# Kernel optimization log

Hardware: AMD Instinct MI355X
Metric: run time of the kernel (lower is better)

The kernel has to match this reference:

```python
import jax, jax.numpy as jnp
import numpy as np

NUM_HEADS = 16
NUM_KV_HEADS = 4
HEAD_DIM = 128
WINDOW = 1024  # sliding window: key j visible to query i iff 0 <= i - j <= WINDOW
SCALE = 0.08838834764831845  # 1/sqrt(HEAD_DIM)
NEG_INF = -1e30


def setup_inputs() -> dict:
    key = jax.random.key(0)
    k1, k2, k3, k4 = jax.random.split(key, 4)
    B, S = 4, 2048
    T = B * S
    return {
        "q": jax.random.normal(k1, (T, NUM_HEADS * HEAD_DIM), dtype=jnp.float32),
        "k": jax.random.normal(k2, (T, NUM_KV_HEADS * HEAD_DIM), dtype=jnp.float32),
        "v": jax.random.normal(k3, (T, NUM_KV_HEADS * HEAD_DIM), dtype=jnp.float32),
        "sinks": jax.random.normal(k4, (NUM_HEADS,), dtype=jnp.float32),
        "batch": B,
        "seqlen": S,
    }


def reference(q, k, v, sinks, batch, seqlen):
    """Varlen causal sliding-window attention with learnable per-head sink logits.

    Equal-length sequences: total_tokens = batch * seqlen, matching
    cu_seqlens = [0, S, 2S, ...] in flash_attn_varlen_func.
    """
    B, S = batch, seqlen
    g = NUM_HEADS // NUM_KV_HEADS
    q = q.reshape(B, S, NUM_HEADS, HEAD_DIM)
    k = k.reshape(B, S, NUM_KV_HEADS, HEAD_DIM)
    v = v.reshape(B, S, NUM_KV_HEADS, HEAD_DIM)
    # GQA: expand kv heads to match query heads
    k = jnp.repeat(k, g, axis=2)  # [B,S,H,D]
    v = jnp.repeat(v, g, axis=2)

    logits = jnp.einsum("bqhd,bkhd->bhqk", q, k) * SCALE  # [B,H,S,S]

    i = jnp.arange(S)[:, None]
    j = jnp.arange(S)[None, :]
    mask = (j <= i) & ((i - j) <= WINDOW)  # causal + sliding window (left=WINDOW, right=-1)
    logits = jnp.where(mask, logits, NEG_INF)

    # Learnable sink: one extra virtual logit per head, contributing no value.
    sink_col = jnp.broadcast_to(sinks[None, :, None, None], (B, NUM_HEADS, S, 1))
    logits = jnp.concatenate([logits, sink_col], axis=-1)  # [B,H,S,S+1]
    probs = jax.nn.softmax(logits, axis=-1)[..., :S]  # drop sink prob (value = 0)

    o = jnp.einsum("bhqk,bkhd->bqhd", probs, v)  # [B,S,H,D]
    return o.reshape(B * S, NUM_HEADS * HEAD_DIM)
```

## Files before the change

kernel.cpp:

```cpp
#include <hip/hip_runtime.h>
#include <hip/hip_bf16.h>

#define NH    16
#define NKVH  4
#define HD    128
#define WIN   1024
#define SEQ   2048
#define QROW  (NH * HD)
#define KROW  (NKVH * HD)
#define LOG2E 1.4426950408889634f
#define QSC   (0.08838834764831845f * LOG2E)

#define KSTR 136
#define VSTR 36

typedef __attribute__((ext_vector_type(8))) short short8;
typedef __attribute__((ext_vector_type(4))) short short4v;
typedef __attribute__((ext_vector_type(4))) float float4v;

#if __has_builtin(__builtin_amdgcn_mfma_f32_16x16x16bf16_1k)
#define MFMA_PV(a, b, c) __builtin_amdgcn_mfma_f32_16x16x16bf16_1k(a, b, c, 0, 0, 0)
#elif __has_builtin(__builtin_amdgcn_mfma_f32_16x16x16_bf16)
#define MFMA_PV(a, b, c) __builtin_amdgcn_mfma_f32_16x16x16_bf16(a, b, c, 0, 0, 0)
#else
static __device__ __forceinline__ float4v mfma_pv_fallback(short4v a, short4v b, float4v c) {
    asm volatile("v_mfma_f32_16x16x16_bf16 %0, %1, %2, %0" : "+v"(c) : "v"(a), "v"(b));
    return c;
}
#define MFMA_PV(a, b, c) mfma_pv_fallback(a, b, c)
#endif

__device__ __forceinline__ unsigned int pk2bf(float a, float b) {
    float2 t; t.x = a; t.y = b;
    __hip_bfloat162 h = __float22bfloat162_rn(t);
    union { __hip_bfloat162 h; unsigned int u; } cv;
    cv.h = h;
    return cv.u;
}

__global__ __launch_bounds__(256, 2)
void attn_swa_sink_kernel(const float* __restrict__ qg, const float* __restrict__ kg,
                          const float* __restrict__ vg, const float* __restrict__ sinks,
                          float* __restrict__ og) {
    __shared__ __align__(16) unsigned short Klds[32 * KSTR];
    __shared__ __align__(16) unsigned short Vlds[128 * VSTR];

    const int gid  = blockIdx.x;
    const int xcd  = gid & 7;
    const int rest = gid >> 3;
    const int qt   = rest >> 1;
    const int g    = ((rest & 1) << 3) | xcd;
    const int b    = g >> 2;
    const int kvh  = g & 3;

    const int tid  = threadIdx.x;
    const int wave = tid >> 6;
    const int lane = tid & 63;
    const int l15  = lane & 15;
    const int quad = lane >> 4;
    const int h    = kvh * 4 + wave;
    const int q0   = qt * 32;

    const float* qbase = qg + (size_t)(b * SEQ) * QROW;
    const float* kbase = kg + (size_t)(b * SEQ) * KROW + kvh * HD;
    const float* vbase = vg + (size_t)(b * SEQ) * KROW + kvh * HD;

    short8 qf[2][4];
#pragma unroll
    for (int qs = 0; qs < 2; ++qs) {
        const float* qr = qbase + (size_t)(q0 + qs * 16 + l15) * QROW + h * HD + quad * 8;
#pragma unroll
        for (int c = 0; c < 4; ++c) {
            float4 x = *(const float4*)(qr + c * 32);
            float4 y = *(const float4*)(qr + c * 32 + 4);
            union { unsigned int u[4]; short8 s; } cv;
            cv.u[0] = pk2bf(x.x * QSC, x.y * QSC);
            cv.u[1] = pk2bf(x.z * QSC, x.w * QSC);
            cv.u[2] = pk2bf(y.x * QSC, y.y * QSC);
            cv.u[3] = pk2bf(y.z * QSC, y.w * QSC);
            qf[qs][c] = cv.s;
        }
    }

    const float sinkv = sinks[h] * LOG2E;
    float m_i[2] = { sinkv, sinkv };
    float l_i[2] = { 1.0f, 1.0f };
    float4v accO[2][8];
#pragma unroll
    for (int qs = 0; qs < 2; ++qs)
#pragma unroll
        for (int f = 0; f < 8; ++f) accO[qs][f] = (float4v)0.0f;

    const int krow = tid >> 3, kcg = tid & 7;
    const int vkg  = tid >> 5, vdg = tid & 31;

    int kt0 = q0 - WIN; if (kt0 < 0) kt0 = 0;
    const int kend = q0 + 32;

    float4 kreg[4], vreg[4];
    {
        const float* kr = kbase + (size_t)(kt0 + krow) * KROW + kcg * 16;
        kreg[0] = *(const float4*)(kr + 0);
        kreg[1] = *(const float4*)(kr + 4);
        kreg[2] = *(const float4*)(kr + 8);
        kreg[3] = *(const float4*)(kr + 12);
        const float* vr = vbase + (size_t)(kt0 + vkg * 4) * KROW + vdg * 4;
        vreg[0] = *(const float4*)(vr + 0 * KROW);
        vreg[1] = *(const float4*)(vr + 1 * KROW);
        vreg[2] = *(const float4*)(vr + 2 * KROW);
        vreg[3] = *(const float4*)(vr + 3 * KROW);
    }

    for (int k0 = kt0; k0 < kend; k0 += 32) {
        __syncthreads();
        {
            uint2* kd = (uint2*)&Klds[krow * KSTR + kcg * 16];
#pragma unroll
            for (int i = 0; i < 4; ++i) {
                uint2 w;
                w.x = pk2bf(((const float*)&kreg[i])[0], ((const float*)&kreg[i])[1]);
                w.y = pk2bf(((const float*)&kreg[i])[2], ((const float*)&kreg[i])[3]);
                kd[i] = w;
            }
#pragma unroll
            for (int i = 0; i < 4; ++i) {
                uint2 w;
                w.x = pk2bf(((const float*)&vreg[0])[i], ((const float*)&vreg[1])[i]);
                w.y = pk2bf(((const float*)&vreg[2])[i], ((const float*)&vreg[3])[i]);
                *(uint2*)&Vlds[(vdg * 4 + i) * VSTR + vkg * 4] = w;
            }
        }
        if (k0 + 32 < kend) {
            const float* kr = kbase + (size_t)(k0 + 32 + krow) * KROW + kcg * 16;
            kreg[0] = *(const float4*)(kr + 0);
            kreg[1] = *(const float4*)(kr + 4);
            kreg[2] = *(const float4*)(kr + 8);
            kreg[3] = *(const float4*)(kr + 12);
            const float* vr = vbase + (size_t)(k0 + 32 + vkg * 4) * KROW + vdg * 4;
            vreg[0] = *(const float4*)(vr + 0 * KROW);
            vreg[1] = *(const float4*)(vr + 1 * KROW);
            vreg[2] = *(const float4*)(vr + 2 * KROW);
            vreg[3] = *(const float4*)(vr + 3 * KROW);
        }
        __syncthreads();

        float4v sacc[2][2];
        sacc[0][0] = (float4v)0.0f; sacc[0][1] = (float4v)0.0f;
        sacc[1][0] = (float4v)0.0f; sacc[1][1] = (float4v)0.0f;
#pragma unroll
        for (int c = 0; c < 4; ++c) {
            short8 kf0 = *(const short8*)&Klds[(l15)      * KSTR + c * 32 + quad * 8];
            short8 kf1 = *(const short8*)&Klds[(16 + l15) * KSTR + c * 32 + quad * 8];
            sacc[0][0] = __builtin_amdgcn_mfma_f32_16x16x32_bf16(kf0, qf[0][c], sacc[0][0], 0, 0, 0);
            sacc[0][1] = __builtin_amdgcn_mfma_f32_16x16x32_bf16(kf0, qf[1][c], sacc[0][1], 0, 0, 0);
            sacc[1][0] = __builtin_amdgcn_mfma_f32_16x16x32_bf16(kf1, qf[0][c], sacc[1][0], 0, 0, 0);
            sacc[1][1] = __builtin_amdgcn_mfma_f32_16x16x32_bf16(kf1, qf[1][c], sacc[1][1], 0, 0, 0);
        }

        short4v pf[2][2];
#pragma unroll
        for (int qs = 0; qs < 2; ++qs) {
            const int query = q0 + qs * 16 + l15;
            const bool full = (k0 + 31 <= q0 + qs * 16) && (q0 + qs * 16 + 15 - k0 <= WIN);
            float ps[2][4];
            float mx = -3.0e38f;
            if (full) {
#pragma unroll
                for (int ks = 0; ks < 2; ++ks)
#pragma unroll
                    for (int r = 0; r < 4; ++r) {
                        float s = sacc[ks][qs][r];
                        ps[ks][r] = s;
                        mx = fmaxf(mx, s);
                    }
            } else {
#pragma unroll
                for (int ks = 0; ks < 2; ++ks)
#pragma unroll
                    for (int r = 0; r < 4; ++r) {
                        const int key = k0 + ks * 16 + quad * 4 + r;
                        const unsigned d = (unsigned)(query - key);
                        float s = (d <= WIN) ? sacc[ks][qs][r] : -1.0e30f;
                        ps[ks][r] = s;
                        mx = fmaxf(mx, s);
                    }
            }
            mx = fmaxf(mx, __shfl_xor(mx, 16));
            mx = fmaxf(mx, __shfl_xor(mx, 32));
            const float mold  = m_i[qs];
            const float mnew  = fmaxf(mold, mx);
            const float alpha = exp2f(mold - mnew);
            m_i[qs] = mnew;
            float sum = 0.0f;
#pragma unroll
            for (int ks = 0; ks < 2; ++ks) {
                float p0 = exp2f(ps[ks][0] - mnew);
                float p1 = exp2f(ps[ks][1] - mnew);
                float p2 = exp2f(ps[ks][2] - mnew);
                float p3 = exp2f(ps[ks][3] - mnew);
                sum += (p0 + p1) + (p2 + p3);
                union { unsigned int u[2]; short4v s; } cv;
                cv.u[0] = pk2bf(p0, p1);
                cv.u[1] = pk2bf(p2, p3);
                pf[qs][ks] = cv.s;
            }
            sum += __shfl_xor(sum, 16);
            sum += __shfl_xor(sum, 32);
            l_i[qs] = l_i[qs] * alpha + sum;
#pragma unroll
            for (int r = 0; r < 4; ++r) {
                const float ar = __shfl(alpha, quad * 4 + r);
#pragma unroll
                for (int f = 0; f < 8; ++f) accO[qs][f][r] *= ar;
            }
        }

#pragma unroll
        for (int f = 0; f < 8; ++f) {
#pragma unroll
            for (int ks = 0; ks < 2; ++ks) {
                short4v vf = *(const short4v*)&Vlds[(f * 16 + l15) * VSTR + ks * 16 + quad * 4];
                accO[0][f] = MFMA_PV(pf[0][ks], vf, accO[0][f]);
                accO[1][f] = MFMA_PV(pf[1][ks], vf, accO[1][f]);
            }
        }
    }

    float* obase = og + (size_t)(b * SEQ) * QROW + h * HD;
#pragma unroll
    for (int qs = 0; qs < 2; ++qs) {
#pragma unroll
        for (int r = 0; r < 4; ++r) {
            const float lq  = __shfl(l_i[qs], quad * 4 + r);
            const float inv = __builtin_amdgcn_rcpf(lq);
            float* orow = obase + (size_t)(q0 + qs * 16 + quad * 4 + r) * QROW;
#pragma unroll
            for (int f = 0; f < 8; ++f)
                orow[f * 16 + l15] = accO[qs][f][r] * inv;
        }
    }
}

extern "C" void kernel_launch(void* const* d_in, const int* in_sizes, int n_in,
                              void* d_out, int out_size, void* d_ws, size_t ws_size,
                              hipStream_t stream) {
    const float* q     = (const float*)d_in[0];
    const float* k     = (const float*)d_in[1];
    const float* v     = (const float*)d_in[2];
    const float* sinks = (const float*)d_in[3];
    float* o = (float*)d_out;
    const int B = 4;
    dim3 grid(B * NKVH * (SEQ / 32));
    dim3 block(256);
    attn_swa_sink_kernel<<<grid, block, 0, stream>>>(q, k, v, sinks, o);
}
```

Measured before the change: 259.4 us.

## Pre-convert K/V to bf16 with transposed V and use 16x16x32 PV MFMA

Adds two pre-pass kernels: one converts K to bf16, the other converts V to bf16 and transposes it into a [b,kvh,d,seq] workspace. The attention kernel then loads bf16 tiles directly into LDS, so the fp32 loads, per-tile conversion and scattered V transpose stores that each block repeated disappear. K rows in LDS are permuted so the PV product can use the wider 16x16x32 MFMA. The change also skips the accumulator rescale when no row max changed and raises occupancy to three blocks. The cost is two extra launches and a workspace round trip.

```diff
diff --git a/kernel.cpp b/kernel.cpp
--- a/kernel.cpp
+++ b/kernel.cpp
@@ -6,29 +6,23 @@
 #define HD    128
 #define WIN   1024
 #define SEQ   2048
+#define NB    4
 #define QROW  (NH * HD)
 #define KROW  (NKVH * HD)
 #define LOG2E 1.4426950408889634f
 #define QSC   (0.08838834764831845f * LOG2E)
 
 #define KSTR 136
-#define VSTR 36
+#define VSTR 40
 
 typedef __attribute__((ext_vector_type(8))) short short8;
-typedef __attribute__((ext_vector_type(4))) short short4v;
 typedef __attribute__((ext_vector_type(4))) float float4v;
 
-#if __has_builtin(__builtin_amdgcn_mfma_f32_16x16x16bf16_1k)
-#define MFMA_PV(a, b, c) __builtin_amdgcn_mfma_f32_16x16x16bf16_1k(a, b, c, 0, 0, 0)
-#elif __has_builtin(__builtin_amdgcn_mfma_f32_16x16x16_bf16)
-#define MFMA_PV(a, b, c) __builtin_amdgcn_mfma_f32_16x16x16_bf16(a, b, c, 0, 0, 0)
-#else
-static __device__ __forceinline__ float4v mfma_pv_fallback(short4v a, short4v b, float4v c) {
-    asm volatile("v_mfma_f32_16x16x16_bf16 %0, %1, %2, %0" : "+v"(c) : "v"(a), "v"(b));
-    return c;
-}
-#define MFMA_PV(a, b, c) mfma_pv_fallback(a, b, c)
-#endif
+__device__ __forceinline__ unsigned short f2bf(float f) {
+    unsigned int u = __float_as_uint(f);
+    unsigned int r = (u + 0x7FFFu + ((u >> 16) & 1u)) >> 16;
+    return (unsigned short)r;
+}
 
 __device__ __forceinline__ unsigned int pk2bf(float a, float b) {
     float2 t; t.x = a; t.y = b;
@@ -38,9 +32,54 @@
     return cv.u;
 }
 
-__global__ __launch_bounds__(256, 2)
-void attn_swa_sink_kernel(const float* __restrict__ qg, const float* __restrict__ kg,
-                          const float* __restrict__ vg, const float* __restrict__ sinks,
+__global__ __launch_bounds__(256)
+void cvt_k_kernel(const float* __restrict__ kg, unsigned short* __restrict__ kb) {
+    const size_t idx = ((size_t)blockIdx.x * 256 + threadIdx.x) * 8;
+    float4 a = *(const float4*)(kg + idx);
+    float4 b = *(const float4*)(kg + idx + 4);
+    uint4 w;
+    w.x = pk2bf(a.x, a.y); w.y = pk2bf(a.z, a.w);
+    w.z = pk2bf(b.x, b.y); w.w = pk2bf(b.z, b.w);
+    *(uint4*)(kb + idx) = w;
+}
+
+#define VTSTR 72
+__global__ __launch_bounds__(256)
+void cvt_vt_kernel(const float* __restrict__ vg, unsigned short* __restrict__ vt) {
+    __shared__ unsigned short T[128 * VTSTR];
+    const int blk = blockIdx.x;
+    const int b   = blk >> 7;
+    const int kvh = (blk >> 5) & 3;
+    const int kb  = blk & 31;
+    const int t   = threadIdx.x;
+
+    const int klocal = t >> 2;
+    const int d0     = (t & 3) * 32;
+    const float* src = vg + (size_t)(b * SEQ + kb * 64 + klocal) * KROW + kvh * HD + d0;
+#pragma unroll
+    for (int c = 0; c < 8; ++c) {
+        float4 x = *(const float4*)(src + c * 4);
+        T[(d0 + c * 4 + 0) * VTSTR + klocal] = f2bf(x.x);
+        T[(d0 + c * 4 + 1) * VTSTR + klocal] = f2bf(x.y);
+        T[(d0 + c * 4 + 2) * VTSTR + klocal] = f2bf(x.z);
+        T[(d0 + c * 4 + 3) * VTSTR + klocal] = f2bf(x.w);
+    }
+    __syncthreads();
+
+    const int d    = t >> 1;
+    const int half = t & 1;
+    const unsigned short* s = &T[d * VTSTR + half * 32];
+    unsigned short* dst = vt + ((size_t)((b * NKVH + kvh) * HD) + d) * SEQ + kb * 64 + half * 32;
+#pragma unroll
+    for (int c = 0; c < 4; ++c)
+        *(uint4*)(dst + c * 8) = *(const uint4*)(s + c * 8);
+}
+
+__global__ __launch_bounds__(256, 3)
+void attn_swa_sink_kernel(const float* __restrict__ qg,
+                          const unsigned short* __restrict__ kb,
+                          const unsigned short* __restrict__ vt,
+                          const float* __restrict__ sinks,
                           float* __restrict__ og) {
     __shared__ __align__(16) unsigned short Klds[32 * KSTR];
     __shared__ __align__(16) unsigned short Vlds[128 * VSTR];
@@ -62,8 +101,8 @@
     const int q0   = qt * 32;
 
     const float* qbase = qg + (size_t)(b * SEQ) * QROW;
-    const float* kbase = kg + (size_t)(b * SEQ) * KROW + kvh * HD;
-    const float* vbase = vg + (size_t)(b * SEQ) * KROW + kvh * HD;
+    const unsigned short* kbase = kb + (size_t)(b * SEQ) * KROW + kvh * HD;
+    const unsigned short* vtbase = vt + (size_t)((b * NKVH + kvh) * HD) * SEQ;
 
     short8 qf[2][4];
 #pragma unroll
@@ -91,56 +130,36 @@
 #pragma unroll
         for (int f = 0; f < 8; ++f) accO[qs][f] = (float4v)0.0f;
 
-    const int krow = tid >> 3, kcg = tid & 7;
-    const int vkg  = tid >> 5, vdg = tid & 31;
+    const int kr  = tid >> 3, kcg = tid & 7;
+    const int lrow = ((kr & 1) << 4) | (kr >> 1);
+    const int vd  = tid >> 1, vh = tid & 1;
 
     int kt0 = q0 - WIN; if (kt0 < 0) kt0 = 0;
     const int kend = q0 + 32;
 
-    float4 kreg[4], vreg[4];
+    uint4 kpre0, kpre1, vpre0, vpre1;
     {
-        const float* kr = kbase + (size_t)(kt0 + krow) * KROW + kcg * 16;
-        kreg[0] = *(const float4*)(kr + 0);
-        kreg[1] = *(const float4*)(kr + 4);
-        kreg[2] = *(const float4*)(kr + 8);
-        kreg[3] = *(const float4*)(kr + 12);
-        const float* vr = vbase + (size_t)(kt0 + vkg * 4) * KROW + vdg * 4;
-        vreg[0] = *(const float4*)(vr + 0 * KROW);
-        vreg[1] = *(const float4*)(vr + 1 * KROW);
-        vreg[2] = *(const float4*)(vr + 2 * KROW);
-        vreg[3] = *(const float4*)(vr + 3 * KROW);
+        const unsigned short* kp = kbase + (size_t)(kt0 + kr) * KROW + kcg * 16;
+        kpre0 = *(const uint4*)(kp);
+        kpre1 = *(const uint4*)(kp + 8);
+        const unsigned short* vp = vtbase + (size_t)vd * SEQ + kt0 + vh * 16;
+        vpre0 = *(const uint4*)(vp);
+        vpre1 = *(const uint4*)(vp + 8);
     }
 
     for (int k0 = kt0; k0 < kend; k0 += 32) {
         __syncthreads();
-        {
-            uint2* kd = (uint2*)&Klds[krow * KSTR + kcg * 16];
-#pragma unroll
-            for (int i = 0; i < 4; ++i) {
-                uint2 w;
-                w.x = pk2bf(((const float*)&kreg[i])[0], ((const float*)&kreg[i])[1]);
-                w.y = pk2bf(((const float*)&kreg[i])[2], ((const float*)&kreg[i])[3]);
-                kd[i] = w;
-            }
-#pragma unroll
-            for (int i = 0; i < 4; ++i) {
-                uint2 w;
-                w.x = pk2bf(((const float*)&vreg[0])[i], ((const float*)&vreg[1])[i]);
-                w.y = pk2bf(((const float*)&vreg[2])[i], ((const float*)&vreg[3])[i]);
-                *(uint2*)&Vlds[(vdg * 4 + i) * VSTR + vkg * 4] = w;
-            }
-        }
+        *(uint4*)&Klds[lrow * KSTR + kcg * 16]     = kpre0;
+        *(uint4*)&Klds[lrow * KSTR + kcg * 16 + 8] = kpre1;
+        *(uint4*)&Vlds[vd * VSTR + vh * 16]        = vpre0;
+        *(uint4*)&Vlds[vd * VSTR + vh * 16 + 8]    = vpre1;
         if (k0 + 32 < kend) {
-            const float* kr = kbase + (size_t)(k0 + 32 + krow) * KROW + kcg * 16;
-            kreg[0] = *(const float4*)(kr + 0);
-            kreg[1] = *(const float4*)(kr + 4);
-            kreg[2] = *(const float4*)(kr + 8);
-            kreg[3] = *(const float4*)(kr + 12);
-            const float* vr = vbase + (size_t)(k0 + 32 + vkg * 4) * KROW + vdg * 4;
-            vreg[0] = *(const float4*)(vr + 0 * KROW);
-            vreg[1] = *(const float4*)(vr + 1 * KROW);
-            vreg[2] = *(const float4*)(vr + 2 * KROW);
-            vreg[3] = *(const float4*)(vr + 3 * KROW);
+            const unsigned short* kp = kbase + (size_t)(k0 + 32 + kr) * KROW + kcg * 16;
+            kpre0 = *(const uint4*)(kp);
+            kpre1 = *(const uint4*)(kp + 8);
+            const unsigned short* vp = vtbase + (size_t)vd * SEQ + (k0 + 32) + vh * 16;
+            vpre0 = *(const uint4*)(vp);
+            vpre1 = *(const uint4*)(vp + 8);
         }
         __syncthreads();
 
@@ -157,7 +176,7 @@
             sacc[1][1] = __builtin_amdgcn_mfma_f32_16x16x32_bf16(kf1, qf[1][c], sacc[1][1], 0, 0, 0);
         }
 
-        short4v pf[2][2];
+        short8 pf[2];
 #pragma unroll
         for (int qs = 0; qs < 2; ++qs) {
             const int query = q0 + qs * 16 + l15;
@@ -178,7 +197,7 @@
                 for (int ks = 0; ks < 2; ++ks)
 #pragma unroll
                     for (int r = 0; r < 4; ++r) {
-                        const int key = k0 + ks * 16 + quad * 4 + r;
+                        const int key = k0 + 8 * quad + 2 * r + ks;
                         const unsigned d = (unsigned)(query - key);
                         float s = (d <= WIN) ? sacc[ks][qs][r] : -1.0e30f;
                         ps[ks][r] = s;
@@ -187,42 +206,40 @@
             }
             mx = fmaxf(mx, __shfl_xor(mx, 16));
             mx = fmaxf(mx, __shfl_xor(mx, 32));
-            const float mold  = m_i[qs];
-            const float mnew  = fmaxf(mold, mx);
-            const float alpha = exp2f(mold - mnew);
+            const float mold = m_i[qs];
+            const float mnew = fmaxf(mold, mx);
             m_i[qs] = mnew;
             float sum = 0.0f;
-#pragma unroll
-            for (int ks = 0; ks < 2; ++ks) {
-                float p0 = exp2f(ps[ks][0] - mnew);
-                float p1 = exp2f(ps[ks][1] - mnew);
-                float p2 = exp2f(ps[ks][2] - mnew);
-                float p3 = exp2f(ps[ks][3] - mnew);
-                sum += (p0 + p1) + (p2 + p3);
-                union { unsigned int u[2]; short4v s; } cv;
-                cv.u[0] = pk2bf(p0, p1);
-                cv.u[1] = pk2bf(p2, p3);
-                pf[qs][ks] = cv.s;
+            union { unsigned int u[4]; short8 s; } cv;
+#pragma unroll
+            for (int r = 0; r < 4; ++r) {
+                const float p0 = exp2f(ps[0][r] - mnew);
+                const float p1 = exp2f(ps[1][r] - mnew);
+                sum += p0 + p1;
+                cv.u[r] = pk2bf(p0, p1);
             }
+            pf[qs] = cv.s;
             sum += __shfl_xor(sum, 16);
             sum += __shfl_xor(sum, 32);
-            l_i[qs] = l_i[qs] * alpha + sum;
-#pragma unroll
-            for (int r = 0; r < 4; ++r) {
-                const float ar = __shfl(alpha, quad * 4 + r);
-#pragma unroll
-                for (int f = 0; f < 8; ++f) accO[qs][f][r] *= ar;
+            if (__any(mnew > mold)) {
+                const float alpha = exp2f(mold - mnew);
+                l_i[qs] = l_i[qs] * alpha + sum;
+#pragma unroll
+                for (int r = 0; r < 4; ++r) {
+                    const float ar = __shfl(alpha, quad * 4 + r);
+#pragma unroll
+                    for (int f = 0; f < 8; ++f) accO[qs][f][r] *= ar;
+                }
+            } else {
+                l_i[qs] += sum;
             }
         }
 
 #pragma unroll
         for (int f = 0; f < 8; ++f) {
-#pragma unroll
-            for (int ks = 0; ks < 2; ++ks) {
-                short4v vf = *(const short4v*)&Vlds[(f * 16 + l15) * VSTR + ks * 16 + quad * 4];
-                accO[0][f] = MFMA_PV(pf[0][ks], vf, accO[0][f]);
-                accO[1][f] = MFMA_PV(pf[1][ks], vf, accO[1][f]);
-            }
+            short8 vf = *(const short8*)&Vlds[(f * 16 + l15) * VSTR + quad * 8];
+            accO[0][f] = __builtin_amdgcn_mfma_f32_16x16x32_bf16(pf[0], vf, accO[0][f], 0, 0, 0);
+            accO[1][f] = __builtin_amdgcn_mfma_f32_16x16x32_bf16(pf[1], vf, accO[1][f], 0, 0, 0);
         }
     }
 
@@ -249,8 +266,13 @@
     const float* v     = (const float*)d_in[2];
     const float* sinks = (const float*)d_in[3];
     float* o = (float*)d_out;
-    const int B = 4;
-    dim3 grid(B * NKVH * (SEQ / 32));
-    dim3 block(256);
-    attn_swa_sink_kernel<<<grid, block, 0, stream>>>(q, k, v, sinks, o);
-}
+
+    unsigned short* kb = (unsigned short*)d_ws;
+    unsigned short* vt = kb + (size_t)NB * SEQ * KROW;
+
+    cvt_k_kernel<<<dim3(NB * SEQ * KROW / (256 * 8)), dim3(256), 0, stream>>>(k, kb);
+    cvt_vt_kernel<<<dim3(NB * NKVH * (SEQ / 64)), dim3(256), 0, stream>>>(v, vt);
+
+    attn_swa_sink_kernel<<<dim3(NB * NKVH * (SEQ / 32)), dim3(256), 0, stream>>>(
+        q, kb, vt, sinks, o);
+}
```

After: 244.3 us. 1.06x faster.
